# Kernel optimization log

Hardware: AMD Instinct MI355X
Metric: run time of the kernel (lower is better)

The kernel has to match this reference:

```python
import jax, jax.numpy as jnp
import numpy as np

B, T, D, H = 8, 1024, 1024, 16
HD = D // H  # 64
FF = 4 * D


def setup_inputs() -> dict:
    key = jax.random.key(0)
    ks = jax.random.split(key, 16)
    s = lambda k, shape, scale: (jax.random.normal(k, shape, dtype=jnp.float32) * scale)
    return {
        "x": s(ks[0], (B, T, D), 1.0),
        "ln1_g": jnp.ones((D,), jnp.float32),
        "ln1_b": jnp.zeros((D,), jnp.float32),
        "ln2_g": jnp.ones((D,), jnp.float32),
        "ln2_b": jnp.zeros((D,), jnp.float32),
        "Wq": s(ks[1], (H, D, HD), 0.02), "bq": jnp.zeros((H, HD), jnp.float32),
        "Wk": s(ks[2], (H, D, HD), 0.02), "bk": jnp.zeros((H, HD), jnp.float32),
        "Wv": s(ks[3], (H, D, HD), 0.02), "bv": jnp.zeros((H, HD), jnp.float32),
        "Wo": s(ks[4], (D, D), 0.02), "bo": jnp.zeros((D,), jnp.float32),
        "W1": s(ks[5], (D, FF), 0.02), "b1": jnp.zeros((FF,), jnp.float32),
        "W2": s(ks[6], (FF, D), 0.02), "b2": jnp.zeros((D,), jnp.float32),
    }


def layer_norm(x, g, b, eps=1e-5):
    mu = jnp.mean(x, axis=-1, keepdims=True)
    var = jnp.mean(jnp.square(x - mu), axis=-1, keepdims=True)
    return (x - mu) * jax.lax.rsqrt(var + eps) * g + b


def reference(x, ln1_g, ln1_b, ln2_g, ln2_b, Wq, bq, Wk, bk, Wv, bv, Wo, bo, W1, b1, W2, b2):
    h = layer_norm(x, ln1_g, ln1_b)
    # Per-head Q/K/V projections, batched over heads (equivalent to the
    # Python loop of per-head Linears in the original module).
    q = jnp.einsum("btd,hde->bhte", h, Wq) + bq[None, :, None, :]
    k = jnp.einsum("btd,hde->bhte", h, Wk) + bk[None, :, None, :]
    v = jnp.einsum("btd,hde->bhte", h, Wv) + bv[None, :, None, :]
    scores = jnp.einsum("bhte,bhse->bhts", q, k) / jnp.sqrt(jnp.float32(HD))
    att = jax.nn.softmax(scores, axis=-1)  # no causal mask in source
    ctx = jnp.einsum("bhts,bhse->bhte", att, v)
    # concat heads along feature dim
    ctx = jnp.transpose(ctx, (0, 2, 1, 3)).reshape(B, T, D)
    attn_out = ctx @ Wo + bo
    x = x + attn_out
    h2 = layer_norm(x, ln2_g, ln2_b)
    ff = jax.nn.gelu(h2 @ W1 + b1, approximate=False) @ W2 + b2
    return x + ff
```

## Files before the change

kernel.cpp:

```cpp
#include <hip/hip_runtime.h>
#include <hip/hip_bf16.h>
#include <cstdint>
#include <cstddef>


typedef __bf16 bf16;
typedef __bf16 bf16x8 __attribute__((ext_vector_type(8)));
typedef __bf16 bf16x4 __attribute__((ext_vector_type(4)));
typedef float  f32x4  __attribute__((ext_vector_type(4)));

#define BB    8
#define TT    1024
#define DD    1024
#define HH    16
#define HDIM  64
#define FFD   4096
#define MROWS (BB*TT)

__device__ __forceinline__ void async_ld16(const void* g, void* l) {
  __builtin_amdgcn_global_load_lds(
      (const __attribute__((address_space(1))) uint32_t*)g,
      (__attribute__((address_space(3))) uint32_t*)l, 16, 0, 0);
}

__device__ __forceinline__ float gelu_f(float v) {
  float z = 0.7978845608028654f * (v + 0.044715f * v * v * v);
  z = fminf(fmaxf(z, -9.0f), 9.0f);
  const float e = __expf(-2.0f * z);
  const float th = 1.0f - __fdividef(2.0f * e, 1.0f + e);
  return 0.5f * v * (1.0f + th);
}

__global__ void k_transpose_cast(const float* __restrict__ src, bf16* __restrict__ dst,
                                 int K, int N) {
  __shared__ float tile[32][33];
  const size_t boff = (size_t)blockIdx.z * K * N;
  src += boff; dst += boff;
  const int k0 = blockIdx.y * 32, n0 = blockIdx.x * 32;
  const int tx = threadIdx.x, ty = threadIdx.y;
#pragma unroll
  for (int i = 0; i < 4; ++i)
    tile[ty + i*8][tx] = src[(size_t)(k0 + ty + i*8) * N + n0 + tx];
  __syncthreads();
#pragma unroll
  for (int i = 0; i < 4; ++i)
    dst[(size_t)(n0 + ty + i*8) * K + k0 + tx] = (bf16)tile[tx][ty + i*8];
}

__global__ void k_concat_bias(const float* __restrict__ bq, const float* __restrict__ bk,
                              const float* __restrict__ bv, float* __restrict__ out) {
  int i = blockIdx.x * 256 + threadIdx.x;
  float v = (i < 1024) ? bq[i] : (i < 2048) ? bk[i - 1024] : bv[i - 2048];
  out[i] = v;
}

__global__ void k_transpose_v(const bf16* __restrict__ qkv, bf16* __restrict__ vT) {
  __shared__ bf16 tile[32][33];
  const int bh = blockIdx.z;
  const int b = bh >> 4, h = bh & 15;
  const int t0 = blockIdx.x * 32, e0 = blockIdx.y * 32;
  const int tx = threadIdx.x, ty = threadIdx.y;
  const bf16* src = qkv + (size_t)b * TT * 3072 + 2048 + h * 64;
#pragma unroll
  for (int i = 0; i < 4; ++i)
    tile[ty + i*8][tx] = src[(size_t)(t0 + ty + i*8) * 3072 + e0 + tx];
  __syncthreads();
  bf16* dst = vT + ((size_t)bh * 64 + e0) * TT + t0;
#pragma unroll
  for (int i = 0; i < 4; ++i)
    dst[(size_t)(ty + i*8) * TT + tx] = tile[tx][ty + i*8];
}

__global__ void k_layernorm(const float* __restrict__ x, const float* __restrict__ g,
                            const float* __restrict__ b, bf16* __restrict__ out) {
  const int row = blockIdx.x, tid = threadIdx.x;
  const float* xr = x + (size_t)row * DD;
  f32x4 v = *(const f32x4*)(xr + tid * 4);
  float s  = v[0] + v[1] + v[2] + v[3];
  float ss = v[0]*v[0] + v[1]*v[1] + v[2]*v[2] + v[3]*v[3];
#pragma unroll
  for (int m = 1; m < 64; m <<= 1) { s += __shfl_xor(s, m); ss += __shfl_xor(ss, m); }
  __shared__ float red[8];
  const int wid = tid >> 6;
  if ((tid & 63) == 0) { red[wid*2] = s; red[wid*2+1] = ss; }
  __syncthreads();
  s  = red[0] + red[2] + red[4] + red[6];
  ss = red[1] + red[3] + red[5] + red[7];
  const float mu = s * (1.0f / DD);
  const float var = ss * (1.0f / DD) - mu * mu;
  const float rs = rsqrtf(var + 1e-5f);
  bf16x4 o;
#pragma unroll
  for (int j = 0; j < 4; ++j)
    o[j] = (bf16)((v[j] - mu) * rs * g[tid*4 + j] + b[tid*4 + j]);
  *(bf16x4*)&out[(size_t)row * DD + tid * 4] = o;
}

template<int MODE>
__global__ __launch_bounds__(512, 2)
void k_gemm256(const bf16* __restrict__ A, const bf16* __restrict__ Bt,
               const float* __restrict__ bias, bf16* __restrict__ outb,
               int M, int N, int K) {
  __shared__ __align__(16) bf16 As[2][256 * 64];
  __shared__ __align__(16) bf16 Bs[2][256 * 64];
  const int tid = threadIdx.x;
  const int w = tid >> 6, l = tid & 63;
  const int wm = w >> 2, wn = w & 3;
  const int l15 = l & 15, l4 = l >> 4;

  const int nbx = N >> 8;
  const int nwg = gridDim.x;
  const int cpx = nwg >> 3;
  const int swz = (blockIdx.x & 7) * cpx + (blockIdx.x >> 3);
  const int m0 = (swz / nbx) << 8, n0 = (swz % nbx) << 8;

  f32x4 acc[8][4] = {};

  const int l7 = l15 & 7;
  const int c0 = (l4 ^ l7) * 8;
  const int c1 = ((4 + l4) ^ l7) * 8;
  const bf16* const A00 = &As[0][(wm*128 + l15)*64 + c0];
  const bf16* const A01 = &As[0][(wm*128 + l15)*64 + c1];
  const bf16* const A10 = &As[1][(wm*128 + l15)*64 + c0];
  const bf16* const A11 = &As[1][(wm*128 + l15)*64 + c1];
  const bf16* const B00 = &Bs[0][(wn*64 + l15)*64 + c0];
  const bf16* const B01 = &Bs[0][(wn*64 + l15)*64 + c1];
  const bf16* const B10 = &Bs[1][(wn*64 + l15)*64 + c0];
  const bf16* const B11 = &Bs[1][(wn*64 + l15)*64 + c1];

  const int srow = l >> 3, sch = l & 7;
  const int schx = (sch ^ srow) * 8;
  const bf16* const aG0 = A  + (size_t)(m0 + w*8 + srow) * K + schx;
  const bf16* const aG1 = aG0 + (size_t)64 * K;
  const bf16* const aG2 = aG0 + (size_t)128 * K;
  const bf16* const aG3 = aG0 + (size_t)192 * K;
  const bf16* const bG0 = Bt + (size_t)(n0 + w*8 + srow) * K + schx;
  const bf16* const bG1 = bG0 + (size_t)64 * K;
  const bf16* const bG2 = bG0 + (size_t)128 * K;
  const bf16* const bG3 = bG0 + (size_t)192 * K;
  bf16* const LA0 = (bf16*)As[0] + w*512;
  bf16* const LA1 = (bf16*)As[1] + w*512;
  bf16* const LB0 = (bf16*)Bs[0] + w*512;
  bf16* const LB1 = (bf16*)Bs[1] + w*512;

  const int NT = K >> 6;

#define RD_B(reg, base) { _Pragma("unroll") \
    for (int nf = 0; nf < 4; ++nf) reg[nf] = *(const bf16x8*)((base) + nf*1024); }
#define RD_A(reg, base, mb) { _Pragma("unroll") \
    for (int mf = 0; mf < 4; ++mf) reg[mf] = *(const bf16x8*)((base) + (mb+mf)*1024); }
#define MM(areg, breg, mb) { _Pragma("unroll") \
    for (int mf = 0; mf < 4; ++mf) _Pragma("unroll") \
      for (int nf = 0; nf < 4; ++nf) \
        acc[mb+mf][nf] = __builtin_amdgcn_mfma_f32_16x16x32_bf16(areg[mf], breg[nf], acc[mb+mf][nf], 0, 0, 0); }
#define SGA(off, lb) { async_ld16(aG0 + (off), (lb)+0*64);  async_ld16(aG1 + (off), (lb)+64*64); \
                       async_ld16(aG2 + (off), (lb)+128*64); async_ld16(aG3 + (off), (lb)+192*64); }
#define SGB2a(off, lb) { async_ld16(bG0 + (off), (lb)+0*64);   async_ld16(bG1 + (off), (lb)+64*64); }
#define SGB2b(off, lb) { async_ld16(bG2 + (off), (lb)+128*64); async_ld16(bG3 + (off), (lb)+192*64); }
#define WAIT_LGKM { asm volatile("s_waitcnt lgkmcnt(0)" ::: "memory"); __builtin_amdgcn_sched_barrier(0); }
#define BAR __builtin_amdgcn_s_barrier()

  SGA(0, LA0)  SGB2a(0, LB0) SGB2b(0, LB0)  SGA(64, LA1)
  asm volatile("s_waitcnt vmcnt(4)" ::: "memory");
  __builtin_amdgcn_sched_barrier(0);
  BAR;

  size_t ko = 0;
  for (int T = 0; T < NT; T += 2) {
    const bool nl  = (T + 2 < NT);
    const bool nl2 = (T + 3 < NT);
    bf16x8 b0[4], b1[4], alo[4], ahi[4];

    RD_B(b0, B00) RD_A(alo, A00, 0)
    SGB2a(ko + 64, LB1)
    BAR; WAIT_LGKM;
    __builtin_amdgcn_s_setprio(1); MM(alo, b0, 0) __builtin_amdgcn_s_setprio(0);
    BAR;
    RD_A(ahi, A00, 4)
    SGB2b(ko + 64, LB1)
    BAR; WAIT_LGKM;
    __builtin_amdgcn_s_setprio(1); MM(ahi, b0, 4) __builtin_amdgcn_s_setprio(0);
    BAR;
    RD_B(b1, B01) RD_A(alo, A01, 0) RD_A(ahi, A01, 4)
    BAR; WAIT_LGKM;
    __builtin_amdgcn_s_setprio(1); MM(alo, b1, 0) __builtin_amdgcn_s_setprio(0);
    BAR;
    if (nl) SGA(ko + 128, LA0)
    __builtin_amdgcn_s_setprio(1); MM(ahi, b1, 4) __builtin_amdgcn_s_setprio(0);
    if (nl) { asm volatile("s_waitcnt vmcnt(4)" ::: "memory"); }
    else    { asm volatile("s_waitcnt vmcnt(0)" ::: "memory"); }
    __builtin_amdgcn_sched_barrier(0);
    BAR;

    RD_B(b0, B10) RD_A(alo, A10, 0)
    if (nl) SGB2a(ko + 128, LB0)
    BAR; WAIT_LGKM;
    __builtin_amdgcn_s_setprio(1); MM(alo, b0, 0) __builtin_amdgcn_s_setprio(0);
    BAR;
    RD_A(ahi, A10, 4)
    if (nl) SGB2b(ko + 128, LB0)
    BAR; WAIT_LGKM;
    __builtin_amdgcn_s_setprio(1); MM(ahi, b0, 4) __builtin_amdgcn_s_setprio(0);
    BAR;
    RD_B(b1, B11) RD_A(alo, A11, 0) RD_A(ahi, A11, 4)
    BAR; WAIT_LGKM;
    __builtin_amdgcn_s_setprio(1); MM(alo, b1, 0) __builtin_amdgcn_s_setprio(0);
    BAR;
    if (nl2) SGA(ko + 192, LA1)
    __builtin_amdgcn_s_setprio(1); MM(ahi, b1, 4) __builtin_amdgcn_s_setprio(0);
    if (nl2) { asm volatile("s_waitcnt vmcnt(4)" ::: "memory"); }
    else     { asm volatile("s_waitcnt vmcnt(0)" ::: "memory"); }
    __builtin_amdgcn_sched_barrier(0);
    BAR;

    ko += 128;
  }
#undef RD_B
#undef RD_A
#undef MM
#undef SGA
#undef SGB2a
#undef SGB2b
#undef WAIT_LGKM
#undef BAR

#pragma unroll
  for (int mf = 0; mf < 8; ++mf) {
#pragma unroll
    for (int r = 0; r < 4; ++r) {
      const size_t grow = (size_t)(m0 + wm*128 + mf*16 + l4*4 + r);
      const size_t rowoff = grow * (size_t)N;
#pragma unroll
      for (int nf = 0; nf < 4; ++nf) {
        const int gcol = n0 + wn*64 + nf*16 + l15;
        float v = acc[mf][nf][r] + bias[gcol];
        if constexpr (MODE == 1) v = gelu_f(v);
        outb[rowoff + gcol] = (bf16)v;
      }
    }
  }
}

template<int MODE>
__global__ __launch_bounds__(256)
void k_gemm(const bf16* __restrict__ A, const bf16* __restrict__ Bt,
            const float* __restrict__ bias, const float* __restrict__ res,
            bf16* __restrict__ outb, float* __restrict__ outf,
            int M, int N, int K) {
  __shared__ __align__(16) bf16 As[128 * 64];
  __shared__ __align__(16) bf16 Bs[128 * 64];
  const int tid = threadIdx.x;
  const int w = tid >> 6, l = tid & 63;
  const int wm = w >> 1, wn = w & 1;
  const int l15 = l & 15, l4 = l >> 4;
  const int m0 = blockIdx.y * 128, n0 = blockIdx.x * 128;

  f32x4 acc[4][4] = {};

  const int l7 = l15 & 7;
  const int c0 = (l4 ^ l7) * 8, c1 = ((4 + l4) ^ l7) * 8;
  const bf16* const Ab = &As[(wm*64 + l15)*64];
  const bf16* const Bb = &Bs[(wn*64 + l15)*64];

  const int sr8 = l >> 3, sl7 = l & 7;
  const int schx = (sl7 ^ sr8) * 8;
  const bf16* const gA0 = A  + (size_t)(m0 + w*32 + sr8) * K + schx;
  const bf16* const gA1 = gA0 + (size_t)8 * K;
  const bf16* const gA2 = gA0 + (size_t)16 * K;
  const bf16* const gA3 = gA0 + (size_t)24 * K;
  const bf16* const gB0 = Bt + (size_t)(n0 + w*32 + sr8) * K + schx;
  const bf16* const gB1 = gB0 + (size_t)8 * K;
  const bf16* const gB2 = gB0 + (size_t)16 * K;
  const bf16* const gB3 = gB0 + (size_t)24 * K;
  bf16* const lA = (bf16*)As + w*32*64;
  bf16* const lB = (bf16*)Bs + w*32*64;

  for (int k0 = 0; k0 < K; k0 += 64) {
    async_ld16(gA0 + k0, lA);          async_ld16(gA1 + k0, lA + 8*64);
    async_ld16(gA2 + k0, lA + 16*64);  async_ld16(gA3 + k0, lA + 24*64);
    async_ld16(gB0 + k0, lB);          async_ld16(gB1 + k0, lB + 8*64);
    async_ld16(gB2 + k0, lB + 16*64);  async_ld16(gB3 + k0, lB + 24*64);
    __syncthreads();
#pragma unroll
    for (int kk = 0; kk < 2; ++kk) {
      const int cc = kk ? c1 : c0;
      bf16x8 af[4], bfr[4];
#pragma unroll
      for (int mf = 0; mf < 4; ++mf) af[mf] = *(const bf16x8*)(Ab + mf*1024 + cc);
#pragma unroll
      for (int nf = 0; nf < 4; ++nf) bfr[nf] = *(const bf16x8*)(Bb + nf*1024 + cc);
#pragma unroll
      for (int mf = 0; mf < 4; ++mf)
#pragma unroll
        for (int nf = 0; nf < 4; ++nf)
          acc[mf][nf] = __builtin_amdgcn_mfma_f32_16x16x32_bf16(af[mf], bfr[nf], acc[mf][nf], 0, 0, 0);
    }
    __syncthreads();
  }

#pragma unroll
  for (int mf = 0; mf < 4; ++mf) {
#pragma unroll
    for (int r = 0; r < 4; ++r) {
      const size_t grow = (size_t)(m0 + wm*64 + mf*16 + l4*4 + r);
      const size_t rowoff = grow * (size_t)N;
#pragma unroll
      for (int nf = 0; nf < 4; ++nf) {
        const int gcol = n0 + wn*64 + nf*16 + l15;
        float v = acc[mf][nf][r] + bias[gcol];
        if constexpr (MODE == 1) v = gelu_f(v);
        if constexpr (MODE == 2) {
          v += res[rowoff + gcol];
          outf[rowoff + gcol] = v;
        } else {
          outb[rowoff + gcol] = (bf16)v;
        }
      }
    }
  }
}

__global__ __launch_bounds__(512)
void k_attn(const bf16* __restrict__ qkv, const bf16* __restrict__ vT,
            bf16* __restrict__ ctx) {
  const int tid = threadIdx.x;
  const int w = tid >> 6, l = tid & 63;
  const int l15 = l & 15, l4 = l >> 4;

  const int gid = ((int)blockIdx.x & 7) * 128 + ((int)blockIdx.x >> 3);
  const int qt = gid & 7;
  const int bh = gid >> 3;
  const int h = bh & 15, b = bh >> 4;

  __shared__ __align__(16) bf16 Ks[2][64 * 64];
  __shared__ __align__(16) bf16 Vs[2][64 * 64];
  __shared__ __align__(16) bf16 P[8][16][72];

  const bf16* base = qkv + (size_t)b * TT * 3072;
  const bf16* Qp = base + h * 64;
  const bf16* Kp = base + 1024 + h * 64;
  const bf16* Vtp = vT + (size_t)bh * HDIM * TT;

  const int qrow = qt * 128 + w * 16 + l15;
  bf16x8 qf[2];
  qf[0] = *(const bf16x8*)&Qp[(size_t)qrow * 3072 + l4 * 8];
  qf[1] = *(const bf16x8*)&Qp[(size_t)qrow * 3072 + 32 + l4 * 8];

  f32x4 oacc[4] = {};
  float mrow[4] = {-1e30f, -1e30f, -1e30f, -1e30f};
  float lrow[4] = {0.f, 0.f, 0.f, 0.f};

  const int srow = w * 8 + (l >> 3);
  const int sch = (l & 7) ^ (srow & 7);

  auto stage = [&](int buf, int t) {
    const int kv0 = t * 64;
    async_ld16(Kp + (size_t)(kv0 + srow) * 3072 + sch * 8, &Ks[buf][w * 512]);
    async_ld16(Vtp + (size_t)srow * TT + kv0 + sch * 8, &Vs[buf][w * 512]);
  };

  stage(0, 0);
  for (int t = 0; t < TT / 64; ++t) {
    const int cur = t & 1;
    __syncthreads();
    if (t + 1 < TT / 64) stage(cur ^ 1, t + 1);

    f32x4 sacc[4] = {};
#pragma unroll
    for (int nf = 0; nf < 4; ++nf) {
      const int row = nf*16 + l15;
#pragma unroll
      for (int kk = 0; kk < 2; ++kk) {
        const int ch = (kk*4 + l4) ^ (row & 7);
        bf16x8 kfr = *(const bf16x8*)&Ks[cur][row*64 + ch*8];
        sacc[nf] = __builtin_amdgcn_mfma_f32_16x16x32_bf16(qf[kk], kfr, sacc[nf], 0, 0, 0);
      }
    }
    float mx[4];
    int ok = 1;
#pragma unroll
    for (int r = 0; r < 4; ++r) {
      float m = -1e30f;
#pragma unroll
      for (int nf = 0; nf < 4; ++nf) { sacc[nf][r] *= 0.125f; m = fmaxf(m, sacc[nf][r]); }
      m = fmaxf(m, __shfl_xor(m, 1));
      m = fmaxf(m, __shfl_xor(m, 2));
      m = fmaxf(m, __shfl_xor(m, 4));
      m = fmaxf(m, __shfl_xor(m, 8));
      mx[r] = m;
      ok &= (m <= mrow[r] + 8.0f);
    }
    if (!__all(ok)) {
#pragma unroll
      for (int r = 0; r < 4; ++r) {
        const float mn = fmaxf(mrow[r], mx[r]);
        const float e = __expf(mrow[r] - mn);
        mrow[r] = mn;
        lrow[r] *= e;
#pragma unroll
        for (int nf = 0; nf < 4; ++nf) oacc[nf][r] *= e;
      }
    }
#pragma unroll
    for (int r = 0; r < 4; ++r) {
      float rs = 0.f;
#pragma unroll
      for (int nf = 0; nf < 4; ++nf) {
        const float pv = __expf(sacc[nf][r] - mrow[r]);
        rs += pv;
        P[w][l4*4 + r][l15 + nf*16] = (bf16)pv;
      }
      rs += __shfl_xor(rs, 1); rs += __shfl_xor(rs, 2);
      rs += __shfl_xor(rs, 4); rs += __shfl_xor(rs, 8);
      lrow[r] += rs;
    }
#pragma unroll
    for (int kk = 0; kk < 2; ++kk) {
      bf16x8 pa = *(const bf16x8*)&P[w][l15][kk*32 + l4*8];
#pragma unroll
      for (int nf = 0; nf < 4; ++nf) {
        const int row = nf*16 + l15;
        const int ch = (kk*4 + l4) ^ (row & 7);
        bf16x8 vb = *(const bf16x8*)&Vs[cur][row*64 + ch*8];
        oacc[nf] = __builtin_amdgcn_mfma_f32_16x16x32_bf16(pa, vb, oacc[nf], 0, 0, 0);
      }
    }
  }
  bf16* outp = ctx + ((size_t)b * TT + qt * 128 + w * 16) * DD + h * 64;
#pragma unroll
  for (int nf = 0; nf < 4; ++nf)
#pragma unroll
    for (int r = 0; r < 4; ++r)
      outp[(size_t)(l4*4 + r) * DD + l15 + nf*16] = (bf16)(oacc[nf][r] / lrow[r]);
}

extern "C" void kernel_launch(void* const* d_in, const int* in_sizes, int n_in,
                              void* d_out, int out_size, void* d_ws, size_t ws_size,
                              hipStream_t stream) {
  const float* x     = (const float*)d_in[0];
  const float* ln1_g = (const float*)d_in[1];
  const float* ln1_b = (const float*)d_in[2];
  const float* ln2_g = (const float*)d_in[3];
  const float* ln2_b = (const float*)d_in[4];
  const float* Wq    = (const float*)d_in[5];
  const float* bq    = (const float*)d_in[6];
  const float* Wk    = (const float*)d_in[7];
  const float* bk    = (const float*)d_in[8];
  const float* Wv    = (const float*)d_in[9];
  const float* bv    = (const float*)d_in[10];
  const float* Wo    = (const float*)d_in[11];
  const float* bo    = (const float*)d_in[12];
  const float* W1    = (const float*)d_in[13];
  const float* b1    = (const float*)d_in[14];
  const float* W2    = (const float*)d_in[15];
  const float* b2    = (const float*)d_in[16];
  float* out = (float*)d_out;

  char* ws = (char*)d_ws;
  bf16* h1    = (bf16*)(ws + 0);
  bf16* vT    = (bf16*)(ws + 0);
  bf16* qkv   = (bf16*)(ws + 16777216);
  bf16* ctx   = (bf16*)(ws + 67108864);
  bf16* u     = (bf16*)(ws + 16777216);
  float* x1   = (float*)(ws + 83886080);
  bf16* wtqkv = (bf16*)(ws + 117440512);
  bf16* wot   = (bf16*)(ws + 123731968);
  bf16* w1t   = (bf16*)(ws + 125829120);
  bf16* w2t   = (bf16*)(ws + 134217728);
  float* bqkv = (float*)(ws + 142606336);
  bf16* h2 = h1;

  dim3 tb(32, 8);
  k_transpose_cast<<<dim3(2, 32, 16), tb, 0, stream>>>(Wq, wtqkv, DD, HDIM);
  k_transpose_cast<<<dim3(2, 32, 16), tb, 0, stream>>>(Wk, wtqkv + 1024*1024, DD, HDIM);
  k_transpose_cast<<<dim3(2, 32, 16), tb, 0, stream>>>(Wv, wtqkv + 2048*1024, DD, HDIM);
  k_transpose_cast<<<dim3(32, 32, 1), tb, 0, stream>>>(Wo, wot, DD, DD);
  k_transpose_cast<<<dim3(128, 32, 1), tb, 0, stream>>>(W1, w1t, DD, FFD);
  k_transpose_cast<<<dim3(32, 128, 1), tb, 0, stream>>>(W2, w2t, FFD, DD);
  k_concat_bias<<<dim3(12), 256, 0, stream>>>(bq, bk, bv, bqkv);

  k_layernorm<<<dim3(MROWS), 256, 0, stream>>>(x, ln1_g, ln1_b, h1);

  k_gemm256<0><<<dim3((MROWS/256)*(3072/256)), 512, 0, stream>>>(
      h1, wtqkv, bqkv, qkv, MROWS, 3072, DD);

  k_transpose_v<<<dim3(32, 2, 128), tb, 0, stream>>>(qkv, vT);

  k_attn<<<dim3(1024), 512, 0, stream>>>(qkv, vT, ctx);

  k_gemm<2><<<dim3(8, 64), 256, 0, stream>>>(ctx, wot, bo, x,
                                             nullptr, x1, MROWS, DD, DD);

  k_layernorm<<<dim3(MROWS), 256, 0, stream>>>(x1, ln2_g, ln2_b, h2);

  k_gemm256<1><<<dim3((MROWS/256)*(FFD/256)), 512, 0, stream>>>(
      h2, w1t, b1, u, MROWS, FFD, DD);

  k_gemm<2><<<dim3(8, 64), 256, 0, stream>>>(u, w2t, b2, x1,
                                             nullptr, out, MROWS, DD, FFD);

  (void)in_sizes; (void)n_in; (void)out_size; (void)ws_size;
}
```

Measured before the change: 444.4 us.

## Split-K FF2 onto 256-tile GEMM, fewer GEMM barriers, exp2 attention softmax

The second FFN GEMM now uses the 256x256 async-LDS GEMM kernel split into two K halves. Each half writes a bf16 partial, and a new combine kernel adds both partials plus the bias and residual in fp32. The 256-tile GEMM main loop is restructured to issue all LDS fragment reads up front, using graded lgkmcnt waits and fewer barriers per tile. Attention switches to base-2 exponentials via v_exp_f32 with a pre-scaled log2e factor, hoists the swizzled LDS addresses, and raises wave priority around the MFMA blocks. The risks are extra precision loss from rounding the split-K partials to bf16, and that the partial buffers reuse workspace regions that held earlier intermediates and transposed weights.

```diff
diff --git a/kernel.cpp b/kernel.cpp
--- a/kernel.cpp
+++ b/kernel.cpp
@@ -29,6 +29,10 @@
   const float e = __expf(-2.0f * z);
   const float th = 1.0f - __fdividef(2.0f * e, 1.0f + e);
   return 0.5f * v * (1.0f + th);
+}
+
+__device__ __forceinline__ float exp2_fast(float x) {
+  float r; asm("v_exp_f32 %0, %1" : "=v"(r) : "v"(x)); return r;
 }
 
 __global__ void k_transpose_cast(const float* __restrict__ src, bf16* __restrict__ dst,
@@ -96,17 +100,22 @@
   *(bf16x4*)&out[(size_t)row * DD + tid * 4] = o;
 }
 
-template<int MODE>
+template<int MODE, int SPLITK>
 __global__ __launch_bounds__(512, 2)
 void k_gemm256(const bf16* __restrict__ A, const bf16* __restrict__ Bt,
-               const float* __restrict__ bias, bf16* __restrict__ outb,
-               int M, int N, int K) {
+               const float* __restrict__ bias, bf16* __restrict__ out0,
+               bf16* __restrict__ out1, int M, int N, int Klen, int lda) {
   __shared__ __align__(16) bf16 As[2][256 * 64];
   __shared__ __align__(16) bf16 Bs[2][256 * 64];
   const int tid = threadIdx.x;
   const int w = tid >> 6, l = tid & 63;
   const int wm = w >> 2, wn = w & 3;
   const int l15 = l & 15, l4 = l >> 4;
+
+  const int z = (SPLITK > 1) ? (int)blockIdx.y : 0;
+  const bf16* Az = A + (size_t)z * Klen;
+  const bf16* Bz = Bt + (size_t)z * Klen;
+  bf16* const outp = (z == 0) ? out0 : out1;
 
   const int nbx = N >> 8;
   const int nwg = gridDim.x;
@@ -130,99 +139,78 @@
 
   const int srow = l >> 3, sch = l & 7;
   const int schx = (sch ^ srow) * 8;
-  const bf16* const aG0 = A  + (size_t)(m0 + w*8 + srow) * K + schx;
-  const bf16* const aG1 = aG0 + (size_t)64 * K;
-  const bf16* const aG2 = aG0 + (size_t)128 * K;
-  const bf16* const aG3 = aG0 + (size_t)192 * K;
-  const bf16* const bG0 = Bt + (size_t)(n0 + w*8 + srow) * K + schx;
-  const bf16* const bG1 = bG0 + (size_t)64 * K;
-  const bf16* const bG2 = bG0 + (size_t)128 * K;
-  const bf16* const bG3 = bG0 + (size_t)192 * K;
+  const bf16* const aG0 = Az + (size_t)(m0 + w*8 + srow) * lda + schx;
+  const bf16* const aG1 = aG0 + (size_t)64 * lda;
+  const bf16* const aG2 = aG0 + (size_t)128 * lda;
+  const bf16* const aG3 = aG0 + (size_t)192 * lda;
+  const bf16* const bG0 = Bz + (size_t)(n0 + w*8 + srow) * lda + schx;
+  const bf16* const bG1 = bG0 + (size_t)64 * lda;
+  const bf16* const bG2 = bG0 + (size_t)128 * lda;
+  const bf16* const bG3 = bG0 + (size_t)192 * lda;
   bf16* const LA0 = (bf16*)As[0] + w*512;
   bf16* const LA1 = (bf16*)As[1] + w*512;
   bf16* const LB0 = (bf16*)Bs[0] + w*512;
   bf16* const LB1 = (bf16*)Bs[1] + w*512;
 
-  const int NT = K >> 6;
-
-#define RD_B(reg, base) { _Pragma("unroll") \
-    for (int nf = 0; nf < 4; ++nf) reg[nf] = *(const bf16x8*)((base) + nf*1024); }
-#define RD_A(reg, base, mb) { _Pragma("unroll") \
-    for (int mf = 0; mf < 4; ++mf) reg[mf] = *(const bf16x8*)((base) + (mb+mf)*1024); }
+  const int NT = Klen >> 6;
+
+#define RD4(reg, base, fo) { _Pragma("unroll") \
+    for (int q = 0; q < 4; ++q) reg[q] = *(const bf16x8*)((base) + ((fo)+q)*1024); }
 #define MM(areg, breg, mb) { _Pragma("unroll") \
     for (int mf = 0; mf < 4; ++mf) _Pragma("unroll") \
       for (int nf = 0; nf < 4; ++nf) \
         acc[mb+mf][nf] = __builtin_amdgcn_mfma_f32_16x16x32_bf16(areg[mf], breg[nf], acc[mb+mf][nf], 0, 0, 0); }
-#define SGA(off, lb) { async_ld16(aG0 + (off), (lb)+0*64);  async_ld16(aG1 + (off), (lb)+64*64); \
+#define SGA(off, lb) { async_ld16(aG0 + (off), (lb)+0*64);   async_ld16(aG1 + (off), (lb)+64*64); \
                        async_ld16(aG2 + (off), (lb)+128*64); async_ld16(aG3 + (off), (lb)+192*64); }
-#define SGB2a(off, lb) { async_ld16(bG0 + (off), (lb)+0*64);   async_ld16(bG1 + (off), (lb)+64*64); }
-#define SGB2b(off, lb) { async_ld16(bG2 + (off), (lb)+128*64); async_ld16(bG3 + (off), (lb)+192*64); }
-#define WAIT_LGKM { asm volatile("s_waitcnt lgkmcnt(0)" ::: "memory"); __builtin_amdgcn_sched_barrier(0); }
+#define SGB(off, lb) { async_ld16(bG0 + (off), (lb)+0*64);   async_ld16(bG1 + (off), (lb)+64*64); \
+                       async_ld16(bG2 + (off), (lb)+128*64); async_ld16(bG3 + (off), (lb)+192*64); }
+#define LGKM(n) { asm volatile("s_waitcnt lgkmcnt(" #n ")" ::: "memory"); __builtin_amdgcn_sched_barrier(0); }
+#define VMC(n)  { asm volatile("s_waitcnt vmcnt(" #n ")" ::: "memory"); __builtin_amdgcn_sched_barrier(0); }
 #define BAR __builtin_amdgcn_s_barrier()
-
-  SGA(0, LA0)  SGB2a(0, LB0) SGB2b(0, LB0)  SGA(64, LA1)
-  asm volatile("s_waitcnt vmcnt(4)" ::: "memory");
-  __builtin_amdgcn_sched_barrier(0);
+#define PR1 __builtin_amdgcn_s_setprio(1)
+#define PR0 __builtin_amdgcn_s_setprio(0)
+
+#define TILE(Apc0, Apc1, Bpc0, Bpc1, LBo, LAs, koB, koA, nl, nl2) { \
+    bf16x8 b0[4], b1[4], alo[4], ahi[4], alo1[4], ahi1[4]; \
+    RD4(b0, Bpc0, 0) RD4(alo, Apc0, 0) RD4(ahi, Apc0, 4) \
+    RD4(b1, Bpc1, 0) RD4(alo1, Apc1, 0) \
+    if (nl) SGB(koB, LBo) \
+    LGKM(8); \
+    PR1; MM(alo, b0, 0) MM(ahi, b0, 4) PR0; \
+    RD4(ahi1, Apc1, 4) \
+    LGKM(4); \
+    PR1; MM(alo1, b1, 0) PR0; \
+    LGKM(0); \
+    BAR; \
+    if (nl2) SGA(koA, LAs) \
+    PR1; MM(ahi1, b1, 4) PR0; \
+    if (nl2) { VMC(4); } else { VMC(0); } \
+    BAR; }
+
+  SGA(0, LA0)  SGB(0, LB0)  SGA(64, LA1)
+  VMC(4);
   BAR;
 
   size_t ko = 0;
   for (int T = 0; T < NT; T += 2) {
-    const bool nl  = (T + 2 < NT);
-    const bool nl2 = (T + 3 < NT);
-    bf16x8 b0[4], b1[4], alo[4], ahi[4];
-
-    RD_B(b0, B00) RD_A(alo, A00, 0)
-    SGB2a(ko + 64, LB1)
-    BAR; WAIT_LGKM;
-    __builtin_amdgcn_s_setprio(1); MM(alo, b0, 0) __builtin_amdgcn_s_setprio(0);
-    BAR;
-    RD_A(ahi, A00, 4)
-    SGB2b(ko + 64, LB1)
-    BAR; WAIT_LGKM;
-    __builtin_amdgcn_s_setprio(1); MM(ahi, b0, 4) __builtin_amdgcn_s_setprio(0);
-    BAR;
-    RD_B(b1, B01) RD_A(alo, A01, 0) RD_A(ahi, A01, 4)
-    BAR; WAIT_LGKM;
-    __builtin_amdgcn_s_setprio(1); MM(alo, b1, 0) __builtin_amdgcn_s_setprio(0);
-    BAR;
-    if (nl) SGA(ko + 128, LA0)
-    __builtin_amdgcn_s_setprio(1); MM(ahi, b1, 4) __builtin_amdgcn_s_setprio(0);
-    if (nl) { asm volatile("s_waitcnt vmcnt(4)" ::: "memory"); }
-    else    { asm volatile("s_waitcnt vmcnt(0)" ::: "memory"); }
-    __builtin_amdgcn_sched_barrier(0);
-    BAR;
-
-    RD_B(b0, B10) RD_A(alo, A10, 0)
-    if (nl) SGB2a(ko + 128, LB0)
-    BAR; WAIT_LGKM;
-    __builtin_amdgcn_s_setprio(1); MM(alo, b0, 0) __builtin_amdgcn_s_setprio(0);
-    BAR;
-    RD_A(ahi, A10, 4)
-    if (nl) SGB2b(ko + 128, LB0)
-    BAR; WAIT_LGKM;
-    __builtin_amdgcn_s_setprio(1); MM(ahi, b0, 4) __builtin_amdgcn_s_setprio(0);
-    BAR;
-    RD_B(b1, B11) RD_A(alo, A11, 0) RD_A(ahi, A11, 4)
-    BAR; WAIT_LGKM;
-    __builtin_amdgcn_s_setprio(1); MM(alo, b1, 0) __builtin_amdgcn_s_setprio(0);
-    BAR;
-    if (nl2) SGA(ko + 192, LA1)
-    __builtin_amdgcn_s_setprio(1); MM(ahi, b1, 4) __builtin_amdgcn_s_setprio(0);
-    if (nl2) { asm volatile("s_waitcnt vmcnt(4)" ::: "memory"); }
-    else     { asm volatile("s_waitcnt vmcnt(0)" ::: "memory"); }
-    __builtin_amdgcn_sched_barrier(0);
-    BAR;
-
+    const bool nlA  = true;
+    const bool nl2A = (T + 2 < NT);
+    const bool nlB  = (T + 2 < NT);
+    const bool nl2B = (T + 3 < NT);
+    TILE(A00, A01, B00, B01, LB1, LA0, ko + 64, ko + 128, nlA, nl2A)
+    TILE(A10, A11, B10, B11, LB0, LA1, ko + 128, ko + 192, nlB, nl2B)
     ko += 128;
   }
-#undef RD_B
-#undef RD_A
+#undef TILE
+#undef RD4
 #undef MM
 #undef SGA
-#undef SGB2a
-#undef SGB2b
-#undef WAIT_LGKM
+#undef SGB
+#undef LGKM
+#undef VMC
 #undef BAR
+#undef PR1
+#undef PR0
 
 #pragma unroll
   for (int mf = 0; mf < 8; ++mf) {
@@ -233,12 +221,32 @@
 #pragma unroll
       for (int nf = 0; nf < 4; ++nf) {
         const int gcol = n0 + wn*64 + nf*16 + l15;
-        float v = acc[mf][nf][r] + bias[gcol];
+        float v = acc[mf][nf][r];
+        if constexpr (MODE != 3) v += bias[gcol];
         if constexpr (MODE == 1) v = gelu_f(v);
-        outb[rowoff + gcol] = (bf16)v;
+        outp[rowoff + gcol] = (bf16)v;
       }
     }
   }
+}
+
+__global__ void k_ff2_combine(const bf16* __restrict__ p0, const bf16* __restrict__ p1,
+                              const float* __restrict__ b2, const float* __restrict__ res,
+                              float* __restrict__ out) {
+  const int i = (blockIdx.x * 256 + threadIdx.x) * 8;
+  const int col = i & 1023;
+  bf16x8 a = *(const bf16x8*)(p0 + i);
+  bf16x8 b = *(const bf16x8*)(p1 + i);
+  f32x4 r0 = *(const f32x4*)(res + i);
+  f32x4 r1 = *(const f32x4*)(res + i + 4);
+  f32x4 o0, o1;
+#pragma unroll
+  for (int j = 0; j < 4; ++j) {
+    o0[j] = (float)a[j]   + (float)b[j]   + b2[col + j]     + r0[j];
+    o1[j] = (float)a[j+4] + (float)b[j+4] + b2[col + j + 4] + r1[j];
+  }
+  *(f32x4*)(out + i)     = o0;
+  *(f32x4*)(out + i + 4) = o1;
 }
 
 template<int MODE>
@@ -350,6 +358,9 @@
   float mrow[4] = {-1e30f, -1e30f, -1e30f, -1e30f};
   float lrow[4] = {0.f, 0.f, 0.f, 0.f};
 
+  const int l7 = l15 & 7;
+  const int c0 = (l4 ^ l7) * 8, c1 = ((4 + l4) ^ l7) * 8;
+
   const int srow = w * 8 + (l >> 3);
   const int sch = (l & 7) ^ (srow & 7);
 
@@ -359,42 +370,48 @@
     async_ld16(Vtp + (size_t)srow * TT + kv0 + sch * 8, &Vs[buf][w * 512]);
   };
 
+  const float SCL = 0.125f * 1.44269504f;
+  const float THR = 8.0f * 1.44269504f;
+
   stage(0, 0);
   for (int t = 0; t < TT / 64; ++t) {
     const int cur = t & 1;
     __syncthreads();
     if (t + 1 < TT / 64) stage(cur ^ 1, t + 1);
 
+    const bf16* const Kc = &Ks[cur][l15 * 64];
+    const bf16* const Vc = &Vs[cur][l15 * 64];
+
     f32x4 sacc[4] = {};
+    __builtin_amdgcn_s_setprio(1);
 #pragma unroll
     for (int nf = 0; nf < 4; ++nf) {
-      const int row = nf*16 + l15;
-#pragma unroll
-      for (int kk = 0; kk < 2; ++kk) {
-        const int ch = (kk*4 + l4) ^ (row & 7);
-        bf16x8 kfr = *(const bf16x8*)&Ks[cur][row*64 + ch*8];
-        sacc[nf] = __builtin_amdgcn_mfma_f32_16x16x32_bf16(qf[kk], kfr, sacc[nf], 0, 0, 0);
-      }
-    }
+      bf16x8 k0 = *(const bf16x8*)(Kc + nf*1024 + c0);
+      bf16x8 k1 = *(const bf16x8*)(Kc + nf*1024 + c1);
+      sacc[nf] = __builtin_amdgcn_mfma_f32_16x16x32_bf16(qf[0], k0, sacc[nf], 0, 0, 0);
+      sacc[nf] = __builtin_amdgcn_mfma_f32_16x16x32_bf16(qf[1], k1, sacc[nf], 0, 0, 0);
+    }
+    __builtin_amdgcn_s_setprio(0);
+
     float mx[4];
     int ok = 1;
 #pragma unroll
     for (int r = 0; r < 4; ++r) {
       float m = -1e30f;
 #pragma unroll
-      for (int nf = 0; nf < 4; ++nf) { sacc[nf][r] *= 0.125f; m = fmaxf(m, sacc[nf][r]); }
+      for (int nf = 0; nf < 4; ++nf) { sacc[nf][r] *= SCL; m = fmaxf(m, sacc[nf][r]); }
       m = fmaxf(m, __shfl_xor(m, 1));
       m = fmaxf(m, __shfl_xor(m, 2));
       m = fmaxf(m, __shfl_xor(m, 4));
       m = fmaxf(m, __shfl_xor(m, 8));
       mx[r] = m;
-      ok &= (m <= mrow[r] + 8.0f);
+      ok &= (m <= mrow[r] + THR);
     }
     if (!__all(ok)) {
 #pragma unroll
       for (int r = 0; r < 4; ++r) {
         const float mn = fmaxf(mrow[r], mx[r]);
-        const float e = __expf(mrow[r] - mn);
+        const float e = exp2_fast(mrow[r] - mn);
         mrow[r] = mn;
         lrow[r] *= e;
 #pragma unroll
@@ -406,7 +423,7 @@
       float rs = 0.f;
 #pragma unroll
       for (int nf = 0; nf < 4; ++nf) {
-        const float pv = __expf(sacc[nf][r] - mrow[r]);
+        const float pv = exp2_fast(sacc[nf][r] - mrow[r]);
         rs += pv;
         P[w][l4*4 + r][l15 + nf*16] = (bf16)pv;
       }
@@ -414,17 +431,18 @@
       rs += __shfl_xor(rs, 4); rs += __shfl_xor(rs, 8);
       lrow[r] += rs;
     }
+    __builtin_amdgcn_s_setprio(1);
 #pragma unroll
     for (int kk = 0; kk < 2; ++kk) {
       bf16x8 pa = *(const bf16x8*)&P[w][l15][kk*32 + l4*8];
+      const int cc = kk ? c1 : c0;
 #pragma unroll
       for (int nf = 0; nf < 4; ++nf) {
-        const int row = nf*16 + l15;
-        const int ch = (kk*4 + l4) ^ (row & 7);
-        bf16x8 vb = *(const bf16x8*)&Vs[cur][row*64 + ch*8];
+        bf16x8 vb = *(const bf16x8*)(Vc + nf*1024 + cc);
         oacc[nf] = __builtin_amdgcn_mfma_f32_16x16x32_bf16(pa, vb, oacc[nf], 0, 0, 0);
       }
     }
+    __builtin_amdgcn_s_setprio(0);
   }
   bf16* outp = ctx + ((size_t)b * TT + qt * 128 + w * 16) * DD + h * 64;
 #pragma unroll
@@ -459,11 +477,13 @@
   char* ws = (char*)d_ws;
   bf16* h1    = (bf16*)(ws + 0);
   bf16* vT    = (bf16*)(ws + 0);
+  bf16* p0    = (bf16*)(ws + 0);
   bf16* qkv   = (bf16*)(ws + 16777216);
   bf16* ctx   = (bf16*)(ws + 67108864);
   bf16* u     = (bf16*)(ws + 16777216);
   float* x1   = (float*)(ws + 83886080);
   bf16* wtqkv = (bf16*)(ws + 117440512);
+  bf16* p1    = (bf16*)(ws + 117440512);
   bf16* wot   = (bf16*)(ws + 123731968);
   bf16* w1t   = (bf16*)(ws + 125829120);
   bf16* w2t   = (bf16*)(ws + 134217728);
@@ -481,8 +501,8 @@
 
   k_layernorm<<<dim3(MROWS), 256, 0, stream>>>(x, ln1_g, ln1_b, h1);
 
-  k_gemm256<0><<<dim3((MROWS/256)*(3072/256)), 512, 0, stream>>>(
-      h1, wtqkv, bqkv, qkv, MROWS, 3072, DD);
+  k_gemm256<0, 1><<<dim3((MROWS/256)*(3072/256)), 512, 0, stream>>>(
+      h1, wtqkv, bqkv, qkv, nullptr, MROWS, 3072, DD, DD);
 
   k_transpose_v<<<dim3(32, 2, 128), tb, 0, stream>>>(qkv, vT);
 
@@ -493,11 +513,13 @@
 
   k_layernorm<<<dim3(MROWS), 256, 0, stream>>>(x1, ln2_g, ln2_b, h2);
 
-  k_gemm256<1><<<dim3((MROWS/256)*(FFD/256)), 512, 0, stream>>>(
-      h2, w1t, b1, u, MROWS, FFD, DD);
-
-  k_gemm<2><<<dim3(8, 64), 256, 0, stream>>>(u, w2t, b2, x1,
-                                             nullptr, out, MROWS, DD, FFD);
+  k_gemm256<1, 1><<<dim3((MROWS/256)*(FFD/256)), 512, 0, stream>>>(
+      h2, w1t, b1, u, nullptr, MROWS, FFD, DD, DD);
+
+  k_gemm256<3, 2><<<dim3((MROWS/256)*(DD/256), 2), 512, 0, stream>>>(
+      u, w2t, nullptr, p0, p1, MROWS, DD, FFD/2, FFD);
+
+  k_ff2_combine<<<dim3(MROWS*DD/2048), 256, 0, stream>>>(p0, p1, b2, x1, out);
 
   (void)in_sizes; (void)n_in; (void)out_size; (void)ws_size;
 }
```

After: 470.0 us. 5.8% more time.

## Transpose QK^T in attention and pass P through registers via bpermute

Applied to the files above, without the earlier changes.

The attention kernel now computes S transposed (K as the A operand), so each lane holds one query row's scores. The row max and sum then need only two cross-lane shuffles. The 1/sqrt(d) and log2(e) scaling is folded into Q once, and exp2 uses v_exp_f32 directly. The P matrix is packed to bf16 and rearranged into the PV MFMA operand layout with ds_bpermute instead of a round trip through shared memory. The change also adds s_setprio around the MFMA sections, at the cost of more register traffic, more bpermute ops and slightly different rounding.

```diff
diff --git a/kernel.cpp b/kernel.cpp
--- a/kernel.cpp
+++ b/kernel.cpp
@@ -8,6 +8,7 @@
 typedef __bf16 bf16x8 __attribute__((ext_vector_type(8)));
 typedef __bf16 bf16x4 __attribute__((ext_vector_type(4)));
 typedef float  f32x4  __attribute__((ext_vector_type(4)));
+typedef uint32_t u32x4 __attribute__((ext_vector_type(4)));
 
 #define BB    8
 #define TT    1024
@@ -29,6 +30,14 @@
   const float e = __expf(-2.0f * z);
   const float th = 1.0f - __fdividef(2.0f * e, 1.0f + e);
   return 0.5f * v * (1.0f + th);
+}
+
+__device__ __forceinline__ float exp2_fast(float x) {
+  float r; asm("v_exp_f32 %0, %1" : "=v"(r) : "v"(x)); return r;
+}
+__device__ __forceinline__ uint32_t cvt_pk_bf16(float a, float b) {
+  uint32_t r; asm("v_cvt_pk_bf16_f32 %0, %1, %2" : "=v"(r) : "v"(a), "v"(b));
+  return r;
 }
 
 __global__ void k_transpose_cast(const float* __restrict__ src, bf16* __restrict__ dst,
@@ -334,21 +343,37 @@
 
   __shared__ __align__(16) bf16 Ks[2][64 * 64];
   __shared__ __align__(16) bf16 Vs[2][64 * 64];
-  __shared__ __align__(16) bf16 P[8][16][72];
 
   const bf16* base = qkv + (size_t)b * TT * 3072;
   const bf16* Qp = base + h * 64;
   const bf16* Kp = base + 1024 + h * 64;
   const bf16* Vtp = vT + (size_t)bh * HDIM * TT;
 
+  const float SCL = 0.125f * 1.44269504f;
+  const float THR = 8.0f * 1.44269504f;
+
   const int qrow = qt * 128 + w * 16 + l15;
   bf16x8 qf[2];
-  qf[0] = *(const bf16x8*)&Qp[(size_t)qrow * 3072 + l4 * 8];
-  qf[1] = *(const bf16x8*)&Qp[(size_t)qrow * 3072 + 32 + l4 * 8];
+  {
+    bf16x8 q0 = *(const bf16x8*)&Qp[(size_t)qrow * 3072 + l4 * 8];
+    bf16x8 q1 = *(const bf16x8*)&Qp[(size_t)qrow * 3072 + 32 + l4 * 8];
+#pragma unroll
+    for (int j = 0; j < 8; ++j) {
+      qf[0][j] = (bf16)((float)q0[j] * SCL);
+      qf[1][j] = (bf16)((float)q1[j] * SCL);
+    }
+  }
 
   f32x4 oacc[4] = {};
-  float mrow[4] = {-1e30f, -1e30f, -1e30f, -1e30f};
-  float lrow[4] = {0.f, 0.f, 0.f, 0.f};
+  float mrow = -1e30f;
+  float lrow = 0.f;
+
+  const int l7 = l15 & 7;
+  const int c0 = (l4 ^ l7) * 8, c1 = ((4 + l4) ^ l7) * 8;
+
+  const int aL0 = (((l4 & 1) << 5) + l15) << 2;
+  const int aL1 = aL0 + 64;
+  const bool hi = (l & 32) != 0;
 
   const int srow = w * 8 + (l >> 3);
   const int sch = (l & 7) ^ (srow & 7);
@@ -365,73 +390,101 @@
     __syncthreads();
     if (t + 1 < TT / 64) stage(cur ^ 1, t + 1);
 
+    const bf16* const Kc = &Ks[cur][l15 * 64];
+    const bf16* const Vc = &Vs[cur][l15 * 64];
+
     f32x4 sacc[4] = {};
+    __builtin_amdgcn_s_setprio(1);
 #pragma unroll
     for (int nf = 0; nf < 4; ++nf) {
-      const int row = nf*16 + l15;
-#pragma unroll
-      for (int kk = 0; kk < 2; ++kk) {
-        const int ch = (kk*4 + l4) ^ (row & 7);
-        bf16x8 kfr = *(const bf16x8*)&Ks[cur][row*64 + ch*8];
-        sacc[nf] = __builtin_amdgcn_mfma_f32_16x16x32_bf16(qf[kk], kfr, sacc[nf], 0, 0, 0);
+      bf16x8 k0 = *(const bf16x8*)(Kc + nf*1024 + c0);
+      bf16x8 k1 = *(const bf16x8*)(Kc + nf*1024 + c1);
+      sacc[nf] = __builtin_amdgcn_mfma_f32_16x16x32_bf16(k0, qf[0], sacc[nf], 0, 0, 0);
+      sacc[nf] = __builtin_amdgcn_mfma_f32_16x16x32_bf16(k1, qf[1], sacc[nf], 0, 0, 0);
+    }
+    __builtin_amdgcn_s_setprio(0);
+
+    float m = fmaxf(fmaxf(sacc[0][0], sacc[0][1]), fmaxf(sacc[0][2], sacc[0][3]));
+#pragma unroll
+    for (int nf = 1; nf < 4; ++nf)
+      m = fmaxf(m, fmaxf(fmaxf(sacc[nf][0], sacc[nf][1]), fmaxf(sacc[nf][2], sacc[nf][3])));
+    m = fmaxf(m, __shfl_xor(m, 16));
+    m = fmaxf(m, __shfl_xor(m, 32));
+
+    const int ok = (m <= mrow + THR);
+    if (!__all(ok)) {
+      const float mn = fmaxf(mrow, m);
+      const float e = exp2_fast(mrow - mn);
+      mrow = mn;
+      lrow *= e;
+      const int qb = l4 << 2;
+      float e0 = __shfl(e, qb + 0), e1 = __shfl(e, qb + 1);
+      float e2 = __shfl(e, qb + 2), e3 = __shfl(e, qb + 3);
+#pragma unroll
+      for (int nf = 0; nf < 4; ++nf) {
+        oacc[nf][0] *= e0; oacc[nf][1] *= e1;
+        oacc[nf][2] *= e2; oacc[nf][3] *= e3;
       }
     }
-    float mx[4];
-    int ok = 1;
-#pragma unroll
-    for (int r = 0; r < 4; ++r) {
-      float m = -1e30f;
-#pragma unroll
-      for (int nf = 0; nf < 4; ++nf) { sacc[nf][r] *= 0.125f; m = fmaxf(m, sacc[nf][r]); }
-      m = fmaxf(m, __shfl_xor(m, 1));
-      m = fmaxf(m, __shfl_xor(m, 2));
-      m = fmaxf(m, __shfl_xor(m, 4));
-      m = fmaxf(m, __shfl_xor(m, 8));
-      mx[r] = m;
-      ok &= (m <= mrow[r] + 8.0f);
-    }
-    if (!__all(ok)) {
+
+    float p[4][4];
+    float ls = 0.f;
+    uint32_t pk0[4], pk1[4];
+#pragma unroll
+    for (int nf = 0; nf < 4; ++nf) {
 #pragma unroll
       for (int r = 0; r < 4; ++r) {
-        const float mn = fmaxf(mrow[r], mx[r]);
-        const float e = __expf(mrow[r] - mn);
-        mrow[r] = mn;
-        lrow[r] *= e;
-#pragma unroll
-        for (int nf = 0; nf < 4; ++nf) oacc[nf][r] *= e;
+        p[nf][r] = exp2_fast(sacc[nf][r] - mrow);
+        ls += p[nf][r];
       }
-    }
-#pragma unroll
-    for (int r = 0; r < 4; ++r) {
-      float rs = 0.f;
+      pk0[nf] = cvt_pk_bf16(p[nf][0], p[nf][1]);
+      pk1[nf] = cvt_pk_bf16(p[nf][2], p[nf][3]);
+    }
+    ls += __shfl_xor(ls, 16);
+    ls += __shfl_xor(ls, 32);
+    lrow += ls;
+
+    __builtin_amdgcn_s_setprio(1);
+#pragma unroll
+    for (int kk = 0; kk < 2; ++kk) {
+      const int nfa = 2*kk, nfb = 2*kk + 1;
+      int u0 = __builtin_amdgcn_ds_bpermute(aL0, (int)pk0[nfa]);
+      int u1 = __builtin_amdgcn_ds_bpermute(aL0, (int)pk0[nfb]);
+      int v0 = __builtin_amdgcn_ds_bpermute(aL0, (int)pk1[nfa]);
+      int v1 = __builtin_amdgcn_ds_bpermute(aL0, (int)pk1[nfb]);
+      int x0 = __builtin_amdgcn_ds_bpermute(aL1, (int)pk0[nfa]);
+      int x1 = __builtin_amdgcn_ds_bpermute(aL1, (int)pk0[nfb]);
+      int y0 = __builtin_amdgcn_ds_bpermute(aL1, (int)pk1[nfa]);
+      int y1 = __builtin_amdgcn_ds_bpermute(aL1, (int)pk1[nfb]);
+      u32x4 pw;
+      pw[0] = (uint32_t)(hi ? u1 : u0);
+      pw[1] = (uint32_t)(hi ? v1 : v0);
+      pw[2] = (uint32_t)(hi ? x1 : x0);
+      pw[3] = (uint32_t)(hi ? y1 : y0);
+      bf16x8 pa = __builtin_bit_cast(bf16x8, pw);
+      const int cc = kk ? c1 : c0;
 #pragma unroll
       for (int nf = 0; nf < 4; ++nf) {
-        const float pv = __expf(sacc[nf][r] - mrow[r]);
-        rs += pv;
-        P[w][l4*4 + r][l15 + nf*16] = (bf16)pv;
-      }
-      rs += __shfl_xor(rs, 1); rs += __shfl_xor(rs, 2);
-      rs += __shfl_xor(rs, 4); rs += __shfl_xor(rs, 8);
-      lrow[r] += rs;
-    }
-#pragma unroll
-    for (int kk = 0; kk < 2; ++kk) {
-      bf16x8 pa = *(const bf16x8*)&P[w][l15][kk*32 + l4*8];
-#pragma unroll
-      for (int nf = 0; nf < 4; ++nf) {
-        const int row = nf*16 + l15;
-        const int ch = (kk*4 + l4) ^ (row & 7);
-        bf16x8 vb = *(const bf16x8*)&Vs[cur][row*64 + ch*8];
+        bf16x8 vb = *(const bf16x8*)(Vc + nf*1024 + cc);
         oacc[nf] = __builtin_amdgcn_mfma_f32_16x16x32_bf16(pa, vb, oacc[nf], 0, 0, 0);
       }
     }
-  }
+    __builtin_amdgcn_s_setprio(0);
+  }
+
+  const int qb = l4 << 2;
+  float li0 = 1.0f / __shfl(lrow, qb + 0);
+  float li1 = 1.0f / __shfl(lrow, qb + 1);
+  float li2 = 1.0f / __shfl(lrow, qb + 2);
+  float li3 = 1.0f / __shfl(lrow, qb + 3);
   bf16* outp = ctx + ((size_t)b * TT + qt * 128 + w * 16) * DD + h * 64;
 #pragma unroll
-  for (int nf = 0; nf < 4; ++nf)
-#pragma unroll
-    for (int r = 0; r < 4; ++r)
-      outp[(size_t)(l4*4 + r) * DD + l15 + nf*16] = (bf16)(oacc[nf][r] / lrow[r]);
+  for (int nf = 0; nf < 4; ++nf) {
+    outp[(size_t)(qb + 0) * DD + l15 + nf*16] = (bf16)(oacc[nf][0] * li0);
+    outp[(size_t)(qb + 1) * DD + l15 + nf*16] = (bf16)(oacc[nf][1] * li1);
+    outp[(size_t)(qb + 2) * DD + l15 + nf*16] = (bf16)(oacc[nf][2] * li2);
+    outp[(size_t)(qb + 3) * DD + l15 + nf*16] = (bf16)(oacc[nf][3] * li3);
+  }
 }
 
 extern "C" void kernel_launch(void* const* d_in, const int* in_sizes, int n_in,
```

Measured after the change: 416.5 us. 6.3% less time.
